# Performance work log

Measured on AMD Instinct MI355X. Metric: run time of the kernel, lower is better.

Reference implementation:

```python
import jax, jax.numpy as jnp
import numpy as np
import math

H = 256; NH = 4; HD = H // NH
D_W = 32; D_A = 32; D_V = 32; D_G = 64
EPS = HD * 1e-05           # GroupNorm eps = head_dim * norm_eps
NEG = -math.exp(-0.5)      # decay prefactor
B, Q, T = 2, 8, 512


def setup_inputs() -> dict:
    ks = iter(jax.random.split(jax.random.key(0), 40))
    def n(shape, s=1.0):
        return (jax.random.normal(next(ks), shape) * s).astype(jnp.float32)
    def u(shape, lo, hi):
        return jax.random.uniform(next(ks), shape, jnp.float32, lo, hi)
    inp = {
        'query': n((B, Q, H)),
        'keyval': n((B, T, H)),
        'v_first': n((B * Q, T, H)),
    }
    for name in ('x_r', 'x_w', 'x_k', 'x_v', 'x_a', 'x_g'):
        inp[name] = u((1, 1, H), 0.0, 1.0)
    inp['w0'] = u((1, 1, H), -7.0, -1.0)
    inp['w1'] = n((H, D_W), 0.1); inp['w2'] = n((D_W, H), 0.1)
    inp['a0'] = n((1, 1, H), 0.1); inp['a1'] = n((H, D_A), 0.1); inp['a2'] = n((D_A, H), 0.1)
    inp['v0'] = 1.0 + n((1, 1, H), 0.1); inp['v1'] = n((H, D_V), 0.1); inp['v2'] = n((D_V, H), 0.1)
    inp['g1'] = n((H, D_G), 0.1); inp['g2'] = n((D_G, H), 0.1)
    inp['k_k'] = u((1, 1, H), 0.7, 1.0); inp['k_a'] = u((1, 1, H), 0.8, 1.2)
    inp['r_k'] = n((NH, HD), 0.1)
    s = 1.0 / math.sqrt(H)
    inp['Wr'] = n((H, H), s); inp['Wk'] = n((H, H), 0.1 * s)
    inp['Wv'] = n((H, H), s); inp['Wo'] = n((H, H), s)
    inp['gn_w'] = jnp.ones((H,), jnp.float32); inp['gn_b'] = jnp.zeros((H,), jnp.float32)
    return inp


def _rwkv7_scan(r, w, k, v, a, b):
    # all inputs [EB, T, NH, HD]; RWKV7 / DPLR delta-rule recurrence (chunk & fused give same math):
    #   S_t = S_{t-1} * exp(w_t)[:,None] + k_t v_t^T + b_t (a_t^T S_{t-1})
    #   o_t = r_t^T S_t
    EB = r.shape[0]
    tm = lambda t: jnp.swapaxes(t, 0, 1)  # time-major [T, EB, NH, HD]
    def step(S, inp):
        r_t, w_t, k_t, v_t, a_t, b_t = inp
        aS = jnp.einsum('bhk,bhkv->bhv', a_t, S)
        S = S * jnp.exp(w_t)[..., None] + k_t[..., None] * v_t[..., None, :] + b_t[..., None] * aS[..., None, :]
        o_t = jnp.einsum('bhk,bhkv->bhv', r_t, S)
        return S, o_t
    S0 = jnp.zeros((EB, NH, HD, HD), r.dtype)
    _, o = jax.lax.scan(step, S0, (tm(r), tm(w), tm(k), tm(v), tm(a), tm(b)))
    return jnp.swapaxes(o, 0, 1)  # [EB, T, NH, HD]


def _forward(query, keyval, v_first, x_r, x_w, x_k, x_v, x_a, x_g,
             w0, w1, w2, a0, a1, a2, v0, v1, v2, g1, g2,
             k_k, k_a, r_k, Wr, Wk, Wv, Wo, gn_w, gn_b):
    Bq, Ql, Hd = query.shape
    Tl = keyval.shape[1]
    EB = Bq * Ql
    # cross-product expansion: each query token attends over the full keyval sequence
    eq = jnp.broadcast_to(query[:, :, None, :], (Bq, Ql, Tl, Hd)).reshape(EB, Tl, Hd)
    hs = jnp.broadcast_to(keyval[:, None, :, :], (Bq, Ql, Tl, Hd)).reshape(EB, Tl, Hd)
    xx_cross = eq - hs
    hs_shift = jnp.pad(hs, ((0, 0), (1, 0), (0, 0)))[:, :Tl]  # ZeroPad2d((0,0,1,-1)) token shift
    xx_kv = hs_shift - hs
    xr = hs + xx_cross * x_r; xw = hs + xx_cross * x_w
    xa = hs + xx_cross * x_a; xg = hs + xx_cross * x_g
    xk = hs + xx_kv * x_k;   xv = hs + xx_kv * x_v
    r = xr @ Wr.T
    w = NEG * jax.nn.sigmoid(w0 + jnp.tanh(xw @ w1) @ w2)  # log-decay in (-exp(-0.5), 0)
    k = xk @ Wk.T
    v = xv @ Wv.T
    v = v + (v_first - v) * jax.nn.sigmoid(v0 + (xv @ v1) @ v2)  # layer_idx != 0
    a = jax.nn.sigmoid(a0 + (xa @ a1) @ a2)
    g = jax.nn.sigmoid(xg @ g1) @ g2
    kk = (k * k_k).reshape(EB, Tl, NH, HD)
    kk = kk / jnp.maximum(jnp.linalg.norm(kk, axis=-1, keepdims=True), 1e-12)  # F.normalize
    k = k + (k * (a - 1.0)) * k_a  # addcmul
    r4, w4, k4, a4 = (t.reshape(EB, Tl, NH, HD) for t in (r, w, k, a))
    v4 = v.reshape(EB, Tl, NH, HD)
    o = _rwkv7_scan(r4, w4, k4, v4, -kk, kk * a4)  # [EB, T, NH, HD]
    # GroupNorm(num_groups=NH) over channels = (h d), biased variance
    mu = o.mean(-1, keepdims=True)
    var = o.var(-1, keepdims=True)
    o = ((o - mu) * jax.lax.rsqrt(var + EPS)).reshape(EB, Tl, NH * HD) * gn_w + gn_b
    o = o + ((r4 * k4 * r_k).sum(-1, keepdims=True) * v4).reshape(EB, Tl, NH * HD)
    o = o * g
    o = o[:, -1, :]  # frames is None -> last token
    return o.reshape(Bq, Ql, NH * HD) @ Wo.T


def reference(query, keyval, v_first, x_r, x_w, x_k, x_v, x_a, x_g,
              w0, w1, w2, a0, a1, a2, v0, v1, v2, g1, g2,
              k_k, k_a, r_k, Wr, Wk, Wv, Wo, gn_w, gn_b):
    return _forward(query, keyval, v_first, x_r, x_w, x_k, x_v, x_a, x_g,
                    w0, w1, w2, a0, a1, a2, v0, v1, v2, g1, g2,
                    k_k, k_a, r_k, Wr, Wk, Wv, Wo, gn_w, gn_b)
```

## Files before the change

### kernel.cpp

```cpp
#include <hip/hip_runtime.h>
#include <math.h>

#define Hn 256
#define NHn 4
#define HDn 64
#define DWn 32
#define DAn 32
#define DVn 32
#define DGn 64
#define Bqn 2
#define Qln 8
#define Tln 512
#define EBn 16
#define NC 16
#define NCH 32

__device__ __forceinline__ float sigm(float x) { return 1.0f / (1.0f + expf(-x)); }

__device__ __forceinline__ float wsum64(float v) {
#pragma unroll
    for (int m = 32; m >= 1; m >>= 1) v += __shfl_xor(v, m, 64);
    return v;
}

__global__ void kA(const float* __restrict__ keyval,
                   const float* __restrict__ x_k, const float* __restrict__ x_v,
                   const float* __restrict__ Wk, const float* __restrict__ Wv,
                   const float* __restrict__ v0, const float* __restrict__ v1,
                   const float* __restrict__ v2, const float* __restrict__ k_k,
                   float* __restrict__ k_g, float* __restrict__ kk_g,
                   float* __restrict__ vraw_g, float* __restrict__ sv_g) {
    int bt = blockIdx.x;
    int t = bt & (Tln - 1);
    int c = threadIdx.x;

    __shared__ __align__(16) float xk_s[Hn];
    __shared__ __align__(16) float xv_s[Hn];
    __shared__ float hv_s[DVn];

    float hs = keyval[bt * Hn + c];
    float pv = (t > 0) ? keyval[(bt - 1) * Hn + c] : 0.0f;
    float d = pv - hs;
    xk_s[c] = fmaf(d, x_k[c], hs);
    xv_s[c] = fmaf(d, x_v[c], hs);
    __syncthreads();

    if (c < DVn) {
        float acc = 0.f;
#pragma unroll 8
        for (int j = 0; j < Hn; ++j) acc = fmaf(xv_s[j], v1[j * DVn + c], acc);
        hv_s[c] = acc;
    }

    float kacc = 0.f, vacc = 0.f;
    const float4* xk4 = (const float4*)xk_s;
    const float4* xv4 = (const float4*)xv_s;
    const float4* wk4 = (const float4*)(Wk + c * Hn);
    const float4* wv4 = (const float4*)(Wv + c * Hn);
#pragma unroll 8
    for (int j = 0; j < Hn / 4; ++j) {
        float4 xa = xk4[j], wa = wk4[j];
        kacc += xa.x * wa.x + xa.y * wa.y + xa.z * wa.z + xa.w * wa.w;
        float4 xb = xv4[j], wb = wv4[j];
        vacc += xb.x * wb.x + xb.y * wb.y + xb.z * wb.z + xb.w * wb.w;
    }
    __syncthreads();

    float svacc = v0[c];
#pragma unroll 8
    for (int dd = 0; dd < DVn; ++dd) svacc = fmaf(hv_s[dd], v2[dd * Hn + c], svacc);
    float sv = sigm(svacc);

    float kkraw = kacc * k_k[c];
    float ss = wsum64(kkraw * kkraw);
    float denom = fmaxf(sqrtf(ss), 1e-12f);
    float kk = kkraw / denom;

    int o = bt * Hn + c;
    k_g[o] = kacc;
    kk_g[o] = kk;
    vraw_g[o] = vacc;
    sv_g[o] = sv;
}

__global__ void kB(const float* __restrict__ query, const float* __restrict__ keyval,
                   const float* __restrict__ x_w, const float* __restrict__ x_a,
                   const float* __restrict__ w0, const float* __restrict__ w1,
                   const float* __restrict__ w2, const float* __restrict__ a0,
                   const float* __restrict__ a1, const float* __restrict__ a2,
                   const float* __restrict__ k_a,
                   const float* __restrict__ k_g, const float* __restrict__ kk_g,
                   const float* __restrict__ vraw_g, const float* __restrict__ sv_g,
                   const float* __restrict__ v_first,
                   float4* __restrict__ coef4, float* __restrict__ vt_g) {
    const float NEGC = -0.60653065971263342f;
    int id = blockIdx.x;
    int eb = id >> 9, t = id & (Tln - 1);
    int b = eb >> 3;
    int c = threadIdx.x;

    __shared__ __align__(16) float xw_s[Hn];
    __shared__ __align__(16) float xa_s[Hn];
    __shared__ float hw_s[DWn];
    __shared__ float ha_s[DAn];

    int bt = (b << 9) + t;
    float hs = keyval[bt * Hn + c];
    float q = query[eb * Hn + c];
    float d = q - hs;
    xw_s[c] = fmaf(d, x_w[c], hs);
    xa_s[c] = fmaf(d, x_a[c], hs);
    __syncthreads();

    if (c < DWn) {
        float acc = 0.f;
#pragma unroll 8
        for (int j = 0; j < Hn; ++j) acc = fmaf(xw_s[j], w1[j * DWn + c], acc);
        hw_s[c] = tanhf(acc);
    } else if (c < DWn + DAn) {
        int dd = c - DWn;
        float acc = 0.f;
#pragma unroll 8
        for (int j = 0; j < Hn; ++j) acc = fmaf(xa_s[j], a1[j * DAn + dd], acc);
        ha_s[dd] = acc;
    }
    __syncthreads();

    float wacc = w0[c], aacc = a0[c];
#pragma unroll 8
    for (int dd = 0; dd < DWn; ++dd) {
        wacc = fmaf(hw_s[dd], w2[dd * Hn + c], wacc);
        aacc = fmaf(ha_s[dd], a2[dd * Hn + c], aacc);
    }
    float w = NEGC * sigm(wacc);
    float a = sigm(aacc);

    int obt = bt * Hn + c;
    size_t oet = (size_t)id * Hn + c;
    float kv = k_g[obt];
    float kkv = kk_g[obt];
    float ew = expf(w);
    float km = kv * fmaf(a - 1.0f, k_a[c], 1.0f);
    float ck = kkv * a;
    coef4[oet] = make_float4(ew, km, ck, kkv);

    float vr = vraw_g[obt];
    float sv = sv_g[obt];
    float vf = v_first[oet];
    vt_g[oet] = fmaf(vf - vr, sv, vr);
}

__global__ void kR(const float* __restrict__ query, const float* __restrict__ keyval,
                   const float* __restrict__ x_r, const float* __restrict__ x_g,
                   const float* __restrict__ Wr, const float* __restrict__ g1,
                   const float* __restrict__ g2, const float* __restrict__ r_k,
                   const float4* __restrict__ coef4,
                   float* __restrict__ r_g, float* __restrict__ g_g,
                   float* __restrict__ sh_g) {
    int eb = blockIdx.x;
    int b = eb >> 3;
    int c = threadIdx.x;

    __shared__ __align__(16) float xr_s[Hn];
    __shared__ __align__(16) float xg_s[Hn];
    __shared__ float hg_s[DGn];

    int btl = (b * Tln + (Tln - 1)) * Hn;
    float hs = keyval[btl + c];
    float q = query[eb * Hn + c];
    float d = q - hs;
    xr_s[c] = fmaf(d, x_r[c], hs);
    xg_s[c] = fmaf(d, x_g[c], hs);
    __syncthreads();

    float racc = 0.f;
    {
        const float4* xr4 = (const float4*)xr_s;
        const float4* wr4 = (const float4*)(Wr + c * Hn);
#pragma unroll 8
        for (int j = 0; j < Hn / 4; ++j) {
            float4 xa = xr4[j], wa = wr4[j];
            racc += xa.x * wa.x + xa.y * wa.y + xa.z * wa.z + xa.w * wa.w;
        }
    }

    if (c < DGn) {
        float gacc = 0.f;
#pragma unroll 8
        for (int j = 0; j < Hn; ++j) gacc = fmaf(xg_s[j], g1[j * DGn + c], gacc);
        hg_s[c] = sigm(gacc);
    }
    __syncthreads();

    float gv = 0.f;
#pragma unroll 8
    for (int dd = 0; dd < DGn; ++dd) gv = fmaf(hg_s[dd], g2[dd * Hn + c], gv);

    float kmv = coef4[((size_t)(eb * Tln + (Tln - 1))) * Hn + c].y;
    float part = wsum64(racc * kmv * r_k[c]);

    r_g[eb * Hn + c] = racc;
    g_g[eb * Hn + c] = gv;
    if ((c & 63) == 0) sh_g[eb * NHn + (c >> 6)] = part;
}

__global__ __launch_bounds__(512) void kScan(
    const float4* __restrict__ coef, const float* __restrict__ vt_g,
    const float* __restrict__ r_g, float* __restrict__ o_raw) {
    int blk = blockIdx.x;
    int eb = blk >> 2, h = blk & 3;
    int tid = threadIdx.x;
    int w = tid >> 6, lane = tid & 63;
    int g = lane >> 3, vv = lane & 7;

    __shared__ __align__(16) float4 cs[2][NC][64];
    __shared__ __align__(16) float  vs[2][NC][64];

    const int sm = tid >> 5;
    const int im = tid & 31;
    const size_t gstep0 = ((size_t)eb * Tln) * Hn + h * HDn;

    float4 rcA0, rcA1, rcB0, rcB1;
    float  rvA0, rvA1, rvB0, rvB1;

#define LOADC(SET, CHUNK)                                                     \
    {                                                                         \
        int cc_ = (CHUNK) < NCH ? (CHUNK) : NCH - 1;                          \
        size_t gb_ = gstep0 + (size_t)(cc_ * NC + sm) * Hn;                   \
        rc##SET##0 = coef[gb_ + im];                                          \
        rc##SET##1 = coef[gb_ + im + 32];                                     \
        rv##SET##0 = vt_g[gb_ + im];                                          \
        rv##SET##1 = vt_g[gb_ + im + 32];                                     \
    }

#define STOREC(SET, B)                                                        \
    {                                                                         \
        cs[B][sm][im]      = rc##SET##0;                                      \
        cs[B][sm][im + 32] = rc##SET##1;                                      \
        vs[B][sm][im]      = rv##SET##0;                                      \
        vs[B][sm][im + 32] = rv##SET##1;                                      \
    }

    const int o0 = (g << 3) | ((0 + g) & 7);
    const int o1 = (g << 3) | ((1 + g) & 7);
    const int o2 = (g << 3) | ((2 + g) & 7);
    const int o3 = (g << 3) | ((3 + g) & 7);
    const int o4 = (g << 3) | ((4 + g) & 7);
    const int o5 = (g << 3) | ((5 + g) & 7);
    const int o6 = (g << 3) | ((6 + g) & 7);
    const int o7 = (g << 3) | ((7 + g) & 7);
    const int vslot = (w << 3) | vv;

    float S[8];
#pragma unroll
    for (int i = 0; i < 8; ++i) S[i] = 0.f;

#define COMPUTE(B)                                                            \
    _Pragma("unroll")                                                         \
    for (int s = 0; s < NC; ++s) {                                            \
        float vt = vs[B][s][vslot];                                           \
        float4 c0 = cs[B][s][o0]; float4 c1 = cs[B][s][o1];                   \
        float4 c2 = cs[B][s][o2]; float4 c3 = cs[B][s][o3];                   \
        float4 c4 = cs[B][s][o4]; float4 c5 = cs[B][s][o5];                   \
        float4 c6 = cs[B][s][o6]; float4 c7 = cs[B][s][o7];                   \
        float p0 = c0.w * S[0];  p0 = fmaf(c2.w, S[2], p0);                   \
        float p1 = c1.w * S[1];  p1 = fmaf(c3.w, S[3], p1);                   \
        float p2 = c4.w * S[4];  p2 = fmaf(c6.w, S[6], p2);                   \
        float p3 = c5.w * S[5];  p3 = fmaf(c7.w, S[7], p3);                   \
        float p = (p0 + p1) + (p2 + p3);                                      \
        p += __shfl_xor(p, 8, 64);                                            \
        p += __shfl_xor(p, 16, 64);                                           \
        p += __shfl_xor(p, 32, 64);                                           \
        float naS = -p;                                                       \
        S[0] = fmaf(S[0], c0.x, fmaf(c0.y, vt, c0.z * naS));                  \
        S[1] = fmaf(S[1], c1.x, fmaf(c1.y, vt, c1.z * naS));                  \
        S[2] = fmaf(S[2], c2.x, fmaf(c2.y, vt, c2.z * naS));                  \
        S[3] = fmaf(S[3], c3.x, fmaf(c3.y, vt, c3.z * naS));                  \
        S[4] = fmaf(S[4], c4.x, fmaf(c4.y, vt, c4.z * naS));                  \
        S[5] = fmaf(S[5], c5.x, fmaf(c5.y, vt, c5.z * naS));                  \
        S[6] = fmaf(S[6], c6.x, fmaf(c6.y, vt, c6.z * naS));                  \
        S[7] = fmaf(S[7], c7.x, fmaf(c7.y, vt, c7.z * naS));                  \
    }

    LOADC(A, 0);
    STOREC(A, 0);
    LOADC(B, 1);
    asm volatile("s_waitcnt lgkmcnt(0)" ::: "memory");
    __builtin_amdgcn_s_barrier();

    for (int c = 0; c < NCH; c += 2) {
        COMPUTE(0);
        LOADC(A, c + 2);
        STOREC(B, 1);
        asm volatile("s_waitcnt lgkmcnt(0)" ::: "memory");
        __builtin_amdgcn_s_barrier();
        COMPUTE(1);
        LOADC(B, c + 3);
        STOREC(A, 0);
        asm volatile("s_waitcnt lgkmcnt(0)" ::: "memory");
        __builtin_amdgcn_s_barrier();
    }

    const float* rr = r_g + eb * Hn + h * HDn;
    float op = 0.f;
    op = fmaf(rr[o0], S[0], op);
    op = fmaf(rr[o1], S[1], op);
    op = fmaf(rr[o2], S[2], op);
    op = fmaf(rr[o3], S[3], op);
    op = fmaf(rr[o4], S[4], op);
    op = fmaf(rr[o5], S[5], op);
    op = fmaf(rr[o6], S[6], op);
    op = fmaf(rr[o7], S[7], op);
    op += __shfl_xor(op, 8, 64);
    op += __shfl_xor(op, 16, 64);
    op += __shfl_xor(op, 32, 64);
    if (lane < 8) o_raw[eb * Hn + h * HDn + (w << 3) + lane] = op;

#undef LOADC
#undef STOREC
#undef COMPUTE
}

__global__ void kD(const float* __restrict__ o_raw, const float* __restrict__ gn_w,
                   const float* __restrict__ gn_b, const float* __restrict__ sh_g,
                   const float* __restrict__ vt_g, const float* __restrict__ g_g,
                   const float* __restrict__ Wo, float* __restrict__ out) {
    const float EPSC = 64e-5f;
    int eb = blockIdx.x;
    int c = threadIdx.x;
    __shared__ __align__(16) float o_s[Hn];

    float o = o_raw[eb * Hn + c];
    float mu = wsum64(o) * (1.0f / HDn);
    float dev = o - mu;
    float var = wsum64(dev * dev) * (1.0f / HDn);
    float og = dev * rsqrtf(var + EPSC) * gn_w[c] + gn_b[c];

    float sh = sh_g[eb * NHn + (c >> 6)];
    float vtl = vt_g[((size_t)(eb * Tln + (Tln - 1))) * Hn + c];
    float o2 = fmaf(sh, vtl, og);
    o_s[c] = o2 * g_g[eb * Hn + c];
    __syncthreads();

    float acc = 0.f;
    const float4* o4 = (const float4*)o_s;
    const float4* w4 = (const float4*)(Wo + c * Hn);
#pragma unroll 8
    for (int j = 0; j < Hn / 4; ++j) {
        float4 xa = o4[j], wa = w4[j];
        acc += xa.x * wa.x + xa.y * wa.y + xa.z * wa.z + xa.w * wa.w;
    }
    out[eb * Hn + c] = acc;
}

extern "C" void kernel_launch(void* const* d_in, const int* in_sizes, int n_in,
                              void* d_out, int out_size, void* d_ws, size_t ws_size,
                              hipStream_t stream) {
    const float* query  = (const float*)d_in[0];
    const float* keyval = (const float*)d_in[1];
    const float* v_first= (const float*)d_in[2];
    const float* x_r = (const float*)d_in[3];
    const float* x_w = (const float*)d_in[4];
    const float* x_k = (const float*)d_in[5];
    const float* x_v = (const float*)d_in[6];
    const float* x_a = (const float*)d_in[7];
    const float* x_g = (const float*)d_in[8];
    const float* w0  = (const float*)d_in[9];
    const float* w1  = (const float*)d_in[10];
    const float* w2  = (const float*)d_in[11];
    const float* a0  = (const float*)d_in[12];
    const float* a1  = (const float*)d_in[13];
    const float* a2  = (const float*)d_in[14];
    const float* v0  = (const float*)d_in[15];
    const float* v1  = (const float*)d_in[16];
    const float* v2  = (const float*)d_in[17];
    const float* g1  = (const float*)d_in[18];
    const float* g2  = (const float*)d_in[19];
    const float* k_k = (const float*)d_in[20];
    const float* k_a = (const float*)d_in[21];
    const float* r_k = (const float*)d_in[22];
    const float* Wr  = (const float*)d_in[23];
    const float* Wk  = (const float*)d_in[24];
    const float* Wv  = (const float*)d_in[25];
    const float* Wo  = (const float*)d_in[26];
    const float* gn_w= (const float*)d_in[27];
    const float* gn_b= (const float*)d_in[28];

    float* ws = (float*)d_ws;
    const size_t BTH = (size_t)Bqn * Tln * Hn;
    const size_t ETH = (size_t)EBn * Tln * Hn;

    float4* coef4 = (float4*)ws;
    float* vt_g   = ws + 4 * ETH;
    float* k_g    = ws + 5 * ETH;
    float* kk_g   = ws + 5 * ETH + BTH;
    float* vraw_g = ws + 5 * ETH + 2 * BTH;
    float* sv_g   = ws + 5 * ETH + 3 * BTH;
    float* r_g    = ws + 5 * ETH + 4 * BTH;
    float* g_g    = r_g + EBn * Hn;
    float* sh_g   = g_g + EBn * Hn;
    float* o_raw  = sh_g + EBn * NHn;

    kA<<<Bqn * Tln, Hn, 0, stream>>>(keyval, x_k, x_v, Wk, Wv, v0, v1, v2, k_k,
                                     k_g, kk_g, vraw_g, sv_g);
    kB<<<EBn * Tln, Hn, 0, stream>>>(query, keyval, x_w, x_a, w0, w1, w2, a0, a1, a2,
                                     k_a, k_g, kk_g, vraw_g, sv_g, v_first,
                                     coef4, vt_g);
    kR<<<EBn, Hn, 0, stream>>>(query, keyval, x_r, x_g, Wr, g1, g2, r_k, coef4,
                               r_g, g_g, sh_g);
    kScan<<<EBn * NHn, 512, 0, stream>>>(coef4, vt_g, r_g, o_raw);
    kD<<<EBn, Hn, 0, stream>>>(o_raw, gn_w, gn_b, sh_g, vt_g, g_g, Wo, (float*)d_out);
}
```

Baseline: 444.3 us.

## Split scan value dimension across four blocks per head

The scan kernel now launches four blocks of 128 threads per (batch, head) instead of one 512-thread block, each handling 16 of the 64 value columns. Because the value columns of the state evolve independently, this gives 256 blocks instead of 64, spreading the serial recurrence over more compute units. The price is that every block reloads the full per-step coefficient data (each thread issues 8 float4 loads per chunk), so coefficient traffic rises fourfold.

After: 496.8 us. 11.8% more time.

```diff
diff --git a/kernel.cpp b/kernel.cpp
--- a/kernel.cpp
+++ b/kernel.cpp
@@ -14,6 +14,7 @@
 #define EBn 16
 #define NC 16
 #define NCH 32
+#define VGn 4
 
 __device__ __forceinline__ float sigm(float x) { return 1.0f / (1.0f + expf(-x)); }
 
@@ -204,41 +205,45 @@
     if ((c & 63) == 0) sh_g[eb * NHn + (c >> 6)] = part;
 }
 
-__global__ __launch_bounds__(512) void kScan(
+__global__ __launch_bounds__(128) void kScan(
     const float4* __restrict__ coef, const float* __restrict__ vt_g,
     const float* __restrict__ r_g, float* __restrict__ o_raw) {
     int blk = blockIdx.x;
-    int eb = blk >> 2, h = blk & 3;
+    int eb = blk >> 4, h = (blk >> 2) & 3, vg = blk & 3;
     int tid = threadIdx.x;
     int w = tid >> 6, lane = tid & 63;
     int g = lane >> 3, vv = lane & 7;
 
     __shared__ __align__(16) float4 cs[2][NC][64];
-    __shared__ __align__(16) float  vs[2][NC][64];
-
-    const int sm = tid >> 5;
-    const int im = tid & 31;
+    __shared__ __align__(16) float  vs[2][NC][16];
+
     const size_t gstep0 = ((size_t)eb * Tln) * Hn + h * HDn;
-
-    float4 rcA0, rcA1, rcB0, rcB1;
+    const int srow = lane, soff = w;
+    const int vts = tid >> 4;
+    const int vtc = tid & 15;
+    const int vcol0 = vg * 16;
+
+    float4 rcA[8], rcB[8];
     float  rvA0, rvA1, rvB0, rvB1;
 
 #define LOADC(SET, CHUNK)                                                     \
     {                                                                         \
         int cc_ = (CHUNK) < NCH ? (CHUNK) : NCH - 1;                          \
-        size_t gb_ = gstep0 + (size_t)(cc_ * NC + sm) * Hn;                   \
-        rc##SET##0 = coef[gb_ + im];                                          \
-        rc##SET##1 = coef[gb_ + im + 32];                                     \
-        rv##SET##0 = vt_g[gb_ + im];                                          \
-        rv##SET##1 = vt_g[gb_ + im + 32];                                     \
+        size_t gb_ = gstep0 + (size_t)(cc_ * NC) * Hn;                        \
+        _Pragma("unroll")                                                     \
+        for (int it = 0; it < 8; ++it)                                        \
+            rc##SET[it] = coef[gb_ + (size_t)(2 * it + soff) * Hn + srow];    \
+        rv##SET##0 = vt_g[gb_ + (size_t)vts * Hn + vcol0 + vtc];              \
+        rv##SET##1 = vt_g[gb_ + (size_t)(vts + 8) * Hn + vcol0 + vtc];        \
     }
 
 #define STOREC(SET, B)                                                        \
     {                                                                         \
-        cs[B][sm][im]      = rc##SET##0;                                      \
-        cs[B][sm][im + 32] = rc##SET##1;                                      \
-        vs[B][sm][im]      = rv##SET##0;                                      \
-        vs[B][sm][im + 32] = rv##SET##1;                                      \
+        _Pragma("unroll")                                                     \
+        for (int it = 0; it < 8; ++it)                                        \
+            cs[B][2 * it + soff][srow] = rc##SET[it];                         \
+        vs[B][vts][vtc]     = rv##SET##0;                                     \
+        vs[B][vts + 8][vtc] = rv##SET##1;                                     \
     }
 
     const int o0 = (g << 3) | ((0 + g) & 7);
@@ -314,7 +319,7 @@
     op += __shfl_xor(op, 8, 64);
     op += __shfl_xor(op, 16, 64);
     op += __shfl_xor(op, 32, 64);
-    if (lane < 8) o_raw[eb * Hn + h * HDn + (w << 3) + lane] = op;
+    if (lane < 8) o_raw[eb * Hn + h * HDn + vg * 16 + (w << 3) + lane] = op;
 
 #undef LOADC
 #undef STOREC
@@ -408,6 +413,6 @@
                                      coef4, vt_g);
     kR<<<EBn, Hn, 0, stream>>>(query, keyval, x_r, x_g, Wr, g1, g2, r_k, coef4,
                                r_g, g_g, sh_g);
-    kScan<<<EBn * NHn, 512, 0, stream>>>(coef4, vt_g, r_g, o_raw);
+    kScan<<<EBn * NHn * VGn, 128, 0, stream>>>(coef4, vt_g, r_g, o_raw);
     kD<<<EBn, Hn, 0, stream>>>(o_raw, gn_w, gn_b, sh_g, vt_g, g_g, Wo, (float*)d_out);
 }
```
